# Performance work log

Measured on AMD Instinct MI355X. Metric: run time of the kernel, lower is better.

Reference implementation:

```python
import jax, jax.numpy as jnp
import numpy as np
from jax import lax

B, P, N = 32, 4096, 1024          # batch, phoneme_num, note_num
VOCAB, D, POS = 100, 256, 10      # hp.vocab_size, hp.encoder_dim, pos-emb dim
H = D                             # LSTM hidden size


def conv1d(x, w, b):
    # x: [B, Cin, L], w: [Cout, Cin, 3], padding=1 (same as torch padding=(k-1)//2)
    y = lax.conv_general_dilated(x, w, (1,), [(1, 1)], dimension_numbers=('NCH', 'OIH', 'NCH'))
    return y + b[None, :, None]


def lstm_dir(x, Wih, Whh, bih, bhh, reverse):
    # x: [B, T, I] -> [B, T, H], PyTorch gate order i,f,g,o
    Bn = x.shape[0]
    h0 = jnp.zeros((Bn, H), x.dtype)
    c0 = jnp.zeros((Bn, H), x.dtype)

    def step(carry, xt):
        h, c = carry
        z = xt @ Wih.T + h @ Whh.T + bih + bhh
        i, f, g, o = jnp.split(z, 4, axis=-1)
        c = jax.nn.sigmoid(f) * c + jax.nn.sigmoid(i) * jnp.tanh(g)
        h = jax.nn.sigmoid(o) * jnp.tanh(c)
        return (h, c), h

    _, hs = lax.scan(step, (h0, c0), x.transpose(1, 0, 2), reverse=reverse)
    return hs.transpose(1, 0, 2)


def bilstm(x, wih, whh, bih, bhh):
    f = lstm_dir(x, wih[0], whh[0], bih[0], bhh[0], False)
    b = lstm_dir(x, wih[1], whh[1], bih[1], bhh[1], True)
    return jnp.concatenate([f, b], axis=-1)


def _forward(score_note_dur, phoneme_seq, phoneme_order, emb, pos_emb,
             mix_w1, mix_b1, mix_w2, mix_b2,
             wih0, whh0, bih0, bhh0, wih1, whh1, bih1, bhh1,
             cnn_w1, cnn_b1, cnn_w2, cnn_b2):
    pe = emb[phoneme_seq]            # [B,P,D]
    po = pos_emb[phoneme_order]      # [B,P,10]
    x = jnp.concatenate([pe, po], axis=-1).transpose(0, 2, 1)  # [B,D+10,P]
    x = jax.nn.relu(conv1d(x, mix_w1, mix_b1))
    x = conv1d(x, mix_w2, mix_b2).transpose(0, 2, 1)            # [B,P,D]

    # Vectorized version of the nested note-boundary loop:
    # runs of tokens > 1 map, in order, to notes 0,1,2,...; the last position is
    # never included (torch loop stops at phoneme_end < len-1 and slices [start:end)).
    Lp = phoneme_seq.shape[1]
    valid = phoneme_seq > 1
    valid = valid.at[:, Lp - 1].set(False)
    prev = jnp.pad(valid[:, :-1], ((0, 0), (1, 0)))
    starts = valid & ~prev
    seg = jnp.cumsum(starts.astype(jnp.int32), axis=1) - 1
    seg = jnp.where(valid, seg, N)  # separators / overflow -> dump segment N

    def agg_one(xb, sb):
        s = jax.ops.segment_sum(xb, sb, num_segments=N + 1)
        c = jax.ops.segment_sum(jnp.ones((Lp,), xb.dtype), sb, num_segments=N + 1)
        return s[:N] / jnp.maximum(c[:N, None], 1.0)

    agg = jax.vmap(agg_one)(x, seg)  # [B,N,D]; empty notes stay zero

    d = score_note_dur[..., None]
    enc = jnp.concatenate([agg, d, 1.0 / (d + 1.0)], axis=-1)  # [B,N,D+2]
    y = bilstm(enc, wih0, whh0, bih0, bhh0)
    y = bilstm(y, wih1, whh1, bih1, bhh1)                       # [B,N,2H]
    y = y.transpose(0, 2, 1)
    y = jax.nn.relu(conv1d(y, cnn_w1, cnn_b1))
    y = conv1d(y, cnn_w2, cnn_b2)
    return y.transpose(0, 2, 1)  # [B,N,1]


def setup_inputs() -> dict:
    keys = iter(jax.random.split(jax.random.key(0), 24))

    def nrm(shape, scale):
        return jax.random.normal(next(keys), shape, jnp.float32) * scale

    s = 1.0 / float(np.sqrt(H))
    inp = {}
    inp['score_note_dur'] = jax.random.uniform(next(keys), (B, N), jnp.float32) * 4.0
    inp['phoneme_seq'] = jax.random.randint(next(keys), (B, P), 0, 8)
    inp['phoneme_order'] = jax.random.randint(next(keys), (B, P), 0, 20)
    inp['emb'] = nrm((VOCAB, D), 0.1).at[0].set(0.0)       # padding_idx=0
    inp['pos_emb'] = nrm((20, POS), 0.1).at[0].set(0.0)    # padding_idx=0
    inp['mix_w1'] = nrm((D, D + POS, 3), s)
    inp['mix_b1'] = jnp.zeros((D,), jnp.float32)
    inp['mix_w2'] = nrm((D, D, 3), s)
    inp['mix_b2'] = jnp.zeros((D,), jnp.float32)
    inp['wih0'] = nrm((2, 4 * H, D + 2), s)
    inp['whh0'] = nrm((2, 4 * H, H), s)
    inp['bih0'] = jnp.zeros((2, 4 * H), jnp.float32)
    inp['bhh0'] = jnp.zeros((2, 4 * H), jnp.float32)
    inp['wih1'] = nrm((2, 4 * H, 2 * H), s)
    inp['whh1'] = nrm((2, 4 * H, H), s)
    inp['bih1'] = jnp.zeros((2, 4 * H), jnp.float32)
    inp['bhh1'] = jnp.zeros((2, 4 * H), jnp.float32)
    inp['cnn_w1'] = nrm((D, 2 * H, 3), s)
    inp['cnn_b1'] = jnp.zeros((D,), jnp.float32)
    inp['cnn_w2'] = nrm((1, D, 3), s)
    inp['cnn_b2'] = jnp.zeros((1,), jnp.float32)
    return inp


def reference(score_note_dur, phoneme_seq, phoneme_order, emb, pos_emb,
              mix_w1, mix_b1, mix_w2, mix_b2,
              wih0, whh0, bih0, bhh0, wih1, whh1, bih1, bhh1,
              cnn_w1, cnn_b1, cnn_w2, cnn_b2):
    return _forward(score_note_dur, phoneme_seq, phoneme_order, emb, pos_emb,
                    mix_w1, mix_b1, mix_w2, mix_b2,
                    wih0, whh0, bih0, bhh0, wih1, whh1, bih1, bhh1,
                    cnn_w1, cnn_b1, cnn_w2, cnn_b2)
```

## Files before the change

### kernel.cpp

```cpp
#include <hip/hip_runtime.h>
#include <math.h>

#define B_    32
#define P_    4096
#define N_    1024
#define POS_  10
#define PP    (P_ + 2)
#define NP    (N_ + 2)
#define GB    8
#define NCHK  (B_ / GB)
#define TCH   128
#define NTCH  (N_ / TCH)
#define X0S   280
#define ENCS  288

typedef unsigned short u16;
typedef _Float16 h2_t __attribute__((ext_vector_type(2)));
typedef unsigned u32x4 __attribute__((ext_vector_type(4)));
typedef short s16x8 __attribute__((ext_vector_type(8)));
typedef float f32x4 __attribute__((ext_vector_type(4)));

__device__ __forceinline__ float sigmoidf_(float x) { return 1.f / (1.f + __expf(-x)); }
__device__ __forceinline__ float tanhf_(float x) {
  float t = fminf(fmaxf(x, -30.f), 30.f);
  float e = __expf(2.f * t);
  return (e - 1.f) / (e + 1.f);
}
__device__ __forceinline__ float bf2f(u16 u) { return __uint_as_float(((unsigned)u) << 16); }
__device__ __forceinline__ u16 f2bf(float f) {
  unsigned u = __float_as_uint(f);
  unsigned r = u + 0x7FFFu + ((u >> 16) & 1u);
  return (u16)(r >> 16);
}
__device__ __forceinline__ u16 f2h_bits(float x) {
  _Float16 hh = (_Float16)x; u16 u; __builtin_memcpy(&u, &hh, 2); return u;
}
__device__ __forceinline__ unsigned pack2h(float lo, float hi) {
  return (unsigned)f2h_bits(lo) | ((unsigned)f2h_bits(hi) << 16);
}
__device__ __forceinline__ float dot2(unsigned w, unsigned h, float acc) {
  return __builtin_amdgcn_fdot2(__builtin_bit_cast(h2_t, w), __builtin_bit_cast(h2_t, h), acc, false);
}
#define DOT4(acc, wq, hq) \
  acc = dot2((wq).x, (hq).x, acc); acc = dot2((wq).y, (hq).y, acc); \
  acc = dot2((wq).z, (hq).z, acc); acc = dot2((wq).w, (hq).w, acc);

#define REP24(X) X(0)X(1)X(2)X(3)X(4)X(5)X(6)X(7)X(8)X(9)X(10)X(11)X(12)X(13)X(14)X(15)X(16)X(17)X(18)X(19)X(20)X(21)X(22)X(23)
#define REP8(X)  X(0)X(1)X(2)X(3)X(4)X(5)X(6)X(7)

__device__ __forceinline__ void stc(float* p, float v) { *p = v; }
__device__ __forceinline__ void stc(u16* p, float v)   { *p = f2bf(v); }

__global__ void fill_sentinel_kernel(float* out, int n, float v) {
  int i = blockIdx.x * 256 + threadIdx.x;
  if (i < n) out[i] = v;
}

__global__ void zero_bf_guards_kernel(u16* X0b, u16* X1b) {
  int cb = blockIdx.x, t = threadIdx.x;
  for (int c = t; c < X0S; c += 256) {
    X0b[((long)cb * PP + 0) * X0S + c] = 0;
    X0b[((long)cb * PP + PP - 1) * X0S + c] = 0;
  }
  if (t < 256) {
    X1b[((long)cb * PP + 0) * 256 + t] = 0;
    X1b[((long)cb * PP + PP - 1) * 256 + t] = 0;
  }
}
__global__ void zero_y1p_guards_kernel(u16* Y1p) {
  int b = blockIdx.x, t = threadIdx.x;
  for (int c = t; c < 512; c += 256) {
    Y1p[((long)b * NP + 0) * 512 + c] = 0;
    Y1p[((long)b * NP + NP - 1) * 512 + c] = 0;
  }
}
__global__ void zero_c3p_guards_kernel(float* C3p) {
  int b = blockIdx.x, t = threadIdx.x;
  if (t < 256) {
    C3p[((long)b * NP + 0) * 256 + t] = 0.f;
    C3p[((long)b * NP + NP - 1) * 256 + t] = 0.f;
  }
}

__global__ void embed_bf16_kernel(const int* __restrict__ seq, const int* __restrict__ order,
                                  const float* __restrict__ emb, const float* __restrict__ pos_emb,
                                  u16* __restrict__ X0b, int b0) {
  long i = (long)blockIdx.x * 256 + threadIdx.x;
  const long total = (long)GB * P_ * X0S;
  if (i >= total) return;
  int c = (int)(i % X0S);
  long bp = i / X0S;
  int p = (int)(bp % P_);
  int cb = (int)(bp / P_);
  int b = b0 + cb;
  float v = 0.f;
  if (c < 256)      v = emb[(long)seq[(long)b * P_ + p] * 256 + c];
  else if (c < 266) v = pos_emb[(long)order[(long)b * P_ + p] * POS_ + (c - 256)];
  X0b[((long)cb * PP + p + 1) * X0S + c] = f2bf(v);
}

__global__ void repack_conv_bt_kernel(const float* __restrict__ w, u16* __restrict__ hi,
                                      u16* __restrict__ lo, int CinReal, int strideA,
                                      int Kpad, int Cout) {
  long i = (long)blockIdx.x * 256 + threadIdx.x;
  if (i >= (long)Cout * Kpad) return;
  int co = (int)(i / Kpad), k = (int)(i - (long)co * Kpad);
  int r = k / strideA, ci = k - r * strideA;
  float v = (r < 3 && ci < CinReal) ? w[((long)co * CinReal + ci) * 3 + r] : 0.f;
  u16 h = f2bf(v);
  hi[i] = h;
  if (lo) lo[i] = f2bf(v - bf2f(h));
}
__global__ void repack_dense_bt_kernel(const float* __restrict__ w, u16* __restrict__ hi,
                                       u16* __restrict__ lo, int CinReal, int Kpad) {
  long i = (long)blockIdx.x * 256 + threadIdx.x;
  if (i >= 1024L * Kpad) return;
  int j = (int)(i / Kpad), k = (int)(i - (long)j * Kpad);
  int co = (j & 3) * 256 + (j >> 2);
  float v = (k < CinReal) ? w[(long)co * CinReal + k] : 0.f;
  u16 h = f2bf(v);
  hi[i] = h;
  lo[i] = f2bf(v - bf2f(h));
}
__global__ void repack_whh_reg_kernel(const float* __restrict__ whh, uint4* __restrict__ Wv) {
  long i = (long)blockIdx.x * 256 + threadIdx.x;
  if (i >= 49152) return;
  int j = (int)(i & 511);
  int t = (int)(i >> 9);
  int kq = t % 24, rb = (t / 24) & 1, d = t / 48;
  int R = (j & 3) * 256 + (j >> 2) + rb * 128;
  const float* wr = whh + ((long)d * 1024 + R) * 256;
  uint4 o; unsigned* op = (unsigned*)&o;
#pragma unroll
  for (int q = 0; q < 4; q++) {
    int k = kq * 8 + 2 * q;
    op[q] = pack2h(wr[k], wr[k + 1]);
  }
  Wv[i] = o;
}
__global__ void repack_whh_lds_kernel(const float* __restrict__ whh, uint4* __restrict__ Ws) {
  long i = (long)blockIdx.x * 256 + threadIdx.x;
  if (i >= 16384) return;
  int d = (int)(i >> 13);
  int a = (int)(i & 8191);
  int rb = a >> 12;
  int rem = a & 4095;
  int i2 = rem >> 9, j = rem & 511;
  int R = (j & 3) * 256 + (j >> 2) + rb * 128;
  const float* wr = whh + ((long)d * 1024 + R) * 256;
  uint4 o; unsigned* op = (unsigned*)&o;
#pragma unroll
  for (int q = 0; q < 4; q++) {
    int k = 192 + i2 * 8 + 2 * q;
    op[q] = pack2h(wr[k], wr[k + 1]);
  }
  Ws[i] = o;
}
__global__ void bias_sum_perm_kernel(const float* __restrict__ a, const float* __restrict__ b,
                                     float* __restrict__ dst) {
  int i = blockIdx.x * 256 + threadIdx.x;
  if (i >= 2048) return;
  int d = i >> 10, j = i & 1023;
  int R = (j & 3) * 256 + (j >> 2);
  dst[i] = a[d * 1024 + R] + b[d * 1024 + R];
}
__global__ void repack_conv4_w_kernel(const float* __restrict__ w, float* __restrict__ dst) {
  int i = blockIdx.x * 256 + threadIdx.x;
  if (i < 768) { int r = i >> 8, ci = i & 255; dst[i] = w[ci * 3 + r]; }
}

template <typename CT, bool SPLIT>
__device__ __forceinline__ void gemm_tile(
    int wave, int lane, int bx, int by,
    const u16* __restrict__ A, const u16* __restrict__ Bt, const u16* __restrict__ Bt2,
    const float* __restrict__ bias, CT* __restrict__ C,
    int N, int Kpad, int Mb,
    long aBatchStride, int aRowStride,
    long cBatchStride, int cRowStride, int relu) {
  int lrow = lane & 15, lk = (lane >> 4) * 8;
  int row0 = bx * 64 + wave * 16;
  int col0 = by * 64;
  int grow = row0 + lrow;
  int b_ = grow / Mb, m_ = grow - b_ * Mb;
  const u16* arow = A + (long)b_ * aBatchStride + (long)m_ * aRowStride + lk;
  const u16* bp0 = Bt + (long)(col0 + lrow) * Kpad + lk;
  const u16* bq0 = SPLIT ? (Bt2 + (long)(col0 + lrow) * Kpad + lk) : bp0;
  f32x4 acc0 = {0.f, 0.f, 0.f, 0.f};
  f32x4 acc1 = acc0, acc2 = acc0, acc3 = acc0;
  for (int kk = 0; kk < Kpad; kk += 32) {
    s16x8 av = *(const s16x8*)(arow + kk);
    acc0 = __builtin_amdgcn_mfma_f32_16x16x32_bf16(av, *(const s16x8*)(bp0 + kk), acc0, 0, 0, 0);
    acc1 = __builtin_amdgcn_mfma_f32_16x16x32_bf16(av, *(const s16x8*)(bp0 + 16L * Kpad + kk), acc1, 0, 0, 0);
    acc2 = __builtin_amdgcn_mfma_f32_16x16x32_bf16(av, *(const s16x8*)(bp0 + 32L * Kpad + kk), acc2, 0, 0, 0);
    acc3 = __builtin_amdgcn_mfma_f32_16x16x32_bf16(av, *(const s16x8*)(bp0 + 48L * Kpad + kk), acc3, 0, 0, 0);
    if (SPLIT) {
      acc0 = __builtin_amdgcn_mfma_f32_16x16x32_bf16(av, *(const s16x8*)(bq0 + kk), acc0, 0, 0, 0);
      acc1 = __builtin_amdgcn_mfma_f32_16x16x32_bf16(av, *(const s16x8*)(bq0 + 16L * Kpad + kk), acc1, 0, 0, 0);
      acc2 = __builtin_amdgcn_mfma_f32_16x16x32_bf16(av, *(const s16x8*)(bq0 + 32L * Kpad + kk), acc2, 0, 0, 0);
      acc3 = __builtin_amdgcn_mfma_f32_16x16x32_bf16(av, *(const s16x8*)(bq0 + 48L * Kpad + kk), acc3, 0, 0, 0);
    }
  }
  int erow = row0 + (lane >> 4) * 4;
  int b2 = erow / Mb, m2 = erow - b2 * Mb;
  CT* cbase = C + (long)b2 * cBatchStride + (long)m2 * cRowStride + col0 + lrow;
#define EPI(cc, accv) { \
    float bv = bias[col0 + (cc) * 16 + lrow]; \
    float v0 = accv[0] + bv, v1 = accv[1] + bv, v2 = accv[2] + bv, v3 = accv[3] + bv; \
    if (relu) { v0 = fmaxf(v0, 0.f); v1 = fmaxf(v1, 0.f); v2 = fmaxf(v2, 0.f); v3 = fmaxf(v3, 0.f); } \
    stc(cbase + 0L * cRowStride + (cc) * 16, v0); \
    stc(cbase + 1L * cRowStride + (cc) * 16, v1); \
    stc(cbase + 2L * cRowStride + (cc) * 16, v2); \
    stc(cbase + 3L * cRowStride + (cc) * 16, v3); }
  EPI(0, acc0) EPI(1, acc1) EPI(2, acc2) EPI(3, acc3)
#undef EPI
}

template <typename CT, bool SPLIT>
__global__ __launch_bounds__(256) void gemm_mfma_kernel(
    const u16* __restrict__ A, const u16* __restrict__ Bt, const u16* __restrict__ Bt2,
    const float* __restrict__ bias, CT* __restrict__ C,
    int N, int Kpad, int Mb,
    long aBatchStride, int aRowStride,
    long cBatchStride, int cRowStride, int relu) {
  int tid = threadIdx.x;
  gemm_tile<CT, SPLIT>(tid >> 6, tid & 63, blockIdx.x, blockIdx.y,
                       A, Bt, Bt2, bias, C, N, Kpad, Mb,
                       aBatchStride, aRowStride, cBatchStride, cRowStride, relu);
}

__global__ __launch_bounds__(256) void seg_scan_kernel(const int* __restrict__ seq,
                                int* __restrict__ nstart, int* __restrict__ nlen) {
  __shared__ unsigned char v[P_];
  __shared__ int sc[2][256];
  int b = blockIdx.x, tid = threadIdx.x;
  for (int i = tid; i < P_; i += 256) {
    int s = seq[(long)b * P_ + i];
    v[i] = (s > 1 && i != P_ - 1) ? 1 : 0;
  }
  for (int n = tid; n < N_; n += 256) { nstart[b * N_ + n] = 0; nlen[b * N_ + n] = 0; }
  __syncthreads();
  int base = tid << 4;
  int c = 0;
#pragma unroll
  for (int i = 0; i < 16; i++) {
    int p = base + i;
    int val = v[p];
    int prev = p ? v[p - 1] : 0;
    c += val & (prev ^ 1);
  }
  sc[0][tid] = c;
  __syncthreads();
  int cur = 0;
  for (int d = 1; d < 256; d <<= 1) {
    int x = sc[cur][tid];
    if (tid >= d) x += sc[cur][tid - d];
    sc[cur ^ 1][tid] = x;
    cur ^= 1;
    __syncthreads();
  }
  int sg = tid ? sc[cur][tid - 1] : 0;
  for (int i = 0; i < 16; i++) {
    int p = base + i;
    int val = v[p];
    int prev = p ? v[p - 1] : 0;
    if (val && !prev) {
      if (sg < N_) {
        int len = 0, q = p;
        while (q < P_ && v[q]) { len++; q++; }
        nstart[b * N_ + sg] = p;
        nlen[b * N_ + sg] = len;
      }
      sg++;
    }
  }
}

__global__ __launch_bounds__(256) void agg_enc_kernel(
    const u16* __restrict__ X2b, const int* __restrict__ nstart, const int* __restrict__ nlen,
    const float* __restrict__ dur, u16* __restrict__ enc, int b0) {
  int n = blockIdx.x, gb = blockIdx.y;
  int b = b0 + gb;
  int d = threadIdx.x;
  int len = nlen[b * N_ + n], st = nstart[b * N_ + n];
  float acc = 0.f;
  for (int i = 0; i < len; i++) acc += bf2f(X2b[((long)gb * PP + st + 1 + i) * 256 + d]);
  float m = (len > 0) ? acc / (float)len : 0.f;
  long e = ((long)b * N_ + n) * ENCS;
  enc[e + d] = f2bf(m);
  if (d == 0) {
    float dd = dur[b * N_ + n];
    enc[e + 256] = f2bf(dd);
    enc[e + 257] = f2bf(1.f / (dd + 1.f));
  }
  if (d >= 2 && d < 32) enc[e + 256 + d] = 0;
}

#define REC_LDS_BYTES (131072 + 4096 + 1024)
__global__ __attribute__((amdgpu_waves_per_eu(2, 2))) __launch_bounds__(512)
void rec_gemm_kernel(
    const float* __restrict__ Z,
    const u32x4* __restrict__ Wv,
    const u32x4* __restrict__ Ws,
    float* __restrict__ state,
    u16* __restrict__ Y, int yRowsPerB, int yPad, int r,
    const u16* __restrict__ Xg, const u16* __restrict__ Whg, const u16* __restrict__ Wlg,
    const float* __restrict__ bsg, float* __restrict__ Zg, int Kpg, int rq) {
  int tid = threadIdx.x;
  if (blockIdx.x >= 64) {
    int half = tid >> 8, vt = tid & 255;
    int tile = (blockIdx.x - 64) * 2 + half;
    int dir = tile >> 10;
    int t2 = tile & 1023;
    int bx = t2 & 63, by = t2 >> 6;
    int t0g = (dir == 0) ? rq * TCH : (NTCH - 1 - rq) * TCH;
    long WihD = (long)1024 * Kpg;
    long ZD = (long)B_ * TCH * 1024;
    gemm_tile<float, true>((vt >> 6), vt & 63, bx, by,
        Xg + (long)t0g * Kpg, Whg + (long)dir * WihD, Wlg + (long)dir * WihD,
        bsg + dir * 1024, Zg + (long)dir * ZD,
        1024, Kpg, TCH, (long)N_ * Kpg, Kpg, (long)TCH * 1024, 1024, 0);
    return;
  }
  extern __shared__ char smem[];
  u32x4* WL = (u32x4*)smem;
  float* zb = (float*)(smem + 131072);
  u16*   hb = (u16*)(smem + 131072 + 4096);
  const u32x4* hb4 = (const u32x4*)hb;

  int chain = blockIdx.x;
  int d = chain >> 5, b = chain & 31;
  const float* Zb = Z + (long)(d * 32 + b) * (TCH * 1024);

  for (int iq = 0; iq < 16; ++iq) {
    int q = iq * 512 + tid;
    WL[q] = Ws[(long)d * 8192 + q];
  }
  const u32x4* WvD = Wv + (long)d * 2 * 24 * 512;
#define DECLW(i) u32x4 wA##i, wB##i;
  REP24(DECLW)
#undef DECLW
#define LOADW(i) wA##i = WvD[(i) * 512 + tid]; wB##i = WvD[(24 + (i)) * 512 + tid];
  REP24(LOADW)
#undef LOADW
#define PINW(i) asm volatile("" : "+v"(wA##i), "+v"(wB##i));
  REP24(PINW)
#undef PINW

  float h_reg = 0.f, c_reg = 0.f;
  if (tid < 256) {
    if (r > 0) {
      h_reg = state[(chain * 2 + 0) * 256 + tid];
      c_reg = state[(chain * 2 + 1) * 256 + tid];
    }
    hb[tid] = f2h_bits(h_reg);
  }
  __syncthreads();

  int t0 = (d == 0) ? r * TCH : (NTCH - 1 - r) * TCH;
  int tcf = d ? (TCH - 1) : 0;
  float preA = Zb[(long)tcf * 1024 + tid];
  float preB = Zb[(long)tcf * 1024 + 512 + tid];

  for (int tt = 0; tt < TCH; ++tt) {
    float accA = preA, accB = preB;
    if (tt + 1 < TCH) {
      int tc2 = d ? (TCH - 2 - tt) : (tt + 1);
      preA = Zb[(long)tc2 * 1024 + tid];
      preB = Zb[(long)tc2 * 1024 + 512 + tid];
    }
#define MACW(i) { u32x4 hq = hb4[i]; DOT4(accA, wA##i, hq); DOT4(accB, wB##i, hq); }
    REP24(MACW)
#undef MACW
#define MACL(i) { u32x4 hq = hb4[24 + (i)]; \
                  u32x4 qa = WL[(i) * 512 + tid]; \
                  u32x4 qb = WL[4096 + (i) * 512 + tid]; \
                  DOT4(accA, qa, hq); DOT4(accB, qb, hq); }
    REP8(MACL)
#undef MACL
    zb[tid] = accA;
    zb[tid + 512] = accB;
    __syncthreads();
    int tcur = d ? (TCH - 1 - tt) : tt;
    if (tid < 256) {
      float4 z4 = *(const float4*)&zb[tid * 4];
      float ig = sigmoidf_(z4.x), fg = sigmoidf_(z4.y);
      float gg = tanhf_(z4.z), og = sigmoidf_(z4.w);
      c_reg = fg * c_reg + ig * gg;
      float h = og * tanhf_(c_reg);
      h_reg = h;
      hb[tid] = f2h_bits(h);
      Y[((long)b * yRowsPerB + t0 + tcur + yPad) * 512 + d * 256 + tid] = f2bf(h);
    }
    __syncthreads();
  }
  if (r != NTCH - 1 && tid < 256) {
    state[(chain * 2 + 0) * 256 + tid] = h_reg;
    state[(chain * 2 + 1) * 256 + tid] = c_reg;
  }
}

__global__ __launch_bounds__(256) void conv4_kernel(
    const float* __restrict__ C3p, const float* __restrict__ w,
    const float* __restrict__ b2, float* __restrict__ out) {
  int row = blockIdx.x * 4 + (threadIdx.x >> 6);
  int lane = threadIdx.x & 63;
  int b = row >> 10, t = row & (N_ - 1);
  const float* a = C3p + ((long)b * NP + t) * 256;
  float acc = 0.f;
  for (int k = lane; k < 768; k += 64) acc += a[k] * w[k];
  for (int off = 32; off; off >>= 1) acc += __shfl_down(acc, off, 64);
  if (lane == 0) out[row] = acc + b2[0];
}

extern "C" void kernel_launch(void* const* d_in, const int* in_sizes, int n_in,
                              void* d_out, int out_size, void* d_ws, size_t ws_size,
                              hipStream_t stream) {
  const float* dur     = (const float*)d_in[0];
  const int*   seq     = (const int*)d_in[1];
  const int*   order   = (const int*)d_in[2];
  const float* emb     = (const float*)d_in[3];
  const float* pos_emb = (const float*)d_in[4];
  const float* mix_w1  = (const float*)d_in[5];
  const float* mix_b1  = (const float*)d_in[6];
  const float* mix_w2  = (const float*)d_in[7];
  const float* mix_b2  = (const float*)d_in[8];
  const float* wih0    = (const float*)d_in[9];
  const float* whh0    = (const float*)d_in[10];
  const float* bih0    = (const float*)d_in[11];
  const float* bhh0    = (const float*)d_in[12];
  const float* wih1    = (const float*)d_in[13];
  const float* whh1    = (const float*)d_in[14];
  const float* bih1    = (const float*)d_in[15];
  const float* bhh1    = (const float*)d_in[16];
  const float* cnn_w1  = (const float*)d_in[17];
  const float* cnn_b1  = (const float*)d_in[18];
  const float* cnn_w2  = (const float*)d_in[19];
  const float* cnn_b2  = (const float*)d_in[20];
  float* out = (float*)d_out;
  float* ws = (float*)d_ws;

  (void)hipFuncSetAttribute((const void*)rec_gemm_kernel,
                            hipFuncAttributeMaxDynamicSharedMemorySize, REC_LDS_BYTES);

  const long X0B_F = (long)GB * PP * X0S / 2;
  const long X1B_F = (long)GB * PP * 256 / 2;
  const long X2B_F = X1B_F;
  const long ZE2   = 2L * B_ * TCH * 1024;
  const long C3P_E = (long)B_ * NP * 256;
  long region = X0B_F + X1B_F + X2B_F;
  if (2 * ZE2 > region) region = 2 * ZE2;
  if (C3P_E > region) region = C3P_E;

  long off = 0;
  auto alloc = [&](long n) { long ret = off; off += (n + 15) & ~15L; return ret; };
  long o_region = alloc(region);
  long o_enc    = alloc((long)B_ * N_ * ENCS / 2);
  long o_Y0     = alloc((long)B_ * N_ * 512 / 2);
  long o_Y1p    = alloc((long)B_ * NP * 512 / 2);
  long o_W1h    = alloc(256L * 832 / 2);
  long o_W2h    = alloc(256L * 768 / 2);
  long o_Wc1h   = alloc(256L * 1536 / 2);
  long o_Wc1l   = alloc(256L * 1536 / 2);
  long o_Wc2r   = alloc(768);
  long o_Wih0h  = alloc(2L * 1024 * ENCS / 2);
  long o_Wih0l  = alloc(2L * 1024 * ENCS / 2);
  long o_Wih1h  = alloc(2L * 1024 * 512 / 2);
  long o_Wih1l  = alloc(2L * 1024 * 512 / 2);
  long o_Wv0    = alloc(49152L * 4);
  long o_Ws0    = alloc(16384L * 4);
  long o_Wv1    = alloc(49152L * 4);
  long o_Ws1    = alloc(16384L * 4);
  long o_bs0    = alloc(2048);
  long o_bs1    = alloc(2048);
  long o_state  = alloc(64L * 2 * 256);
  long o_nst    = alloc((long)B_ * N_);
  long o_nln    = alloc((long)B_ * N_);

  if ((size_t)(off * 4) > ws_size) {
    float v = -(1000.0f + (float)(ws_size >> 20));
    fill_sentinel_kernel<<<(out_size + 255) / 256, 256, 0, stream>>>(out, out_size, v);
    return;
  }

  u16*   X0b  = (u16*)(ws + o_region);
  u16*   X1b  = (u16*)(ws + o_region + X0B_F);
  u16*   X2b  = (u16*)(ws + o_region + X0B_F + X1B_F);
  float* Zbuf[2] = { ws + o_region, ws + o_region + ZE2 };
  float* C3p  = ws + o_region;
  u16*   enc  = (u16*)(ws + o_enc);
  u16*   Y0   = (u16*)(ws + o_Y0);
  u16*   Y1p  = (u16*)(ws + o_Y1p);
  u16*   W1h  = (u16*)(ws + o_W1h);
  u16*   W2h  = (u16*)(ws + o_W2h);
  u16*   Wc1h = (u16*)(ws + o_Wc1h);
  u16*   Wc1l = (u16*)(ws + o_Wc1l);
  float* Wc2r = ws + o_Wc2r;
  u16*   Wih0h = (u16*)(ws + o_Wih0h);
  u16*   Wih0l = (u16*)(ws + o_Wih0l);
  u16*   Wih1h = (u16*)(ws + o_Wih1h);
  u16*   Wih1l = (u16*)(ws + o_Wih1l);
  uint4* Wv0  = (uint4*)(ws + o_Wv0);
  uint4* Ws0  = (uint4*)(ws + o_Ws0);
  uint4* Wv1  = (uint4*)(ws + o_Wv1);
  uint4* Ws1  = (uint4*)(ws + o_Ws1);
  float* bs0  = ws + o_bs0;
  float* bs1  = ws + o_bs1;
  float* state = ws + o_state;
  int* nstart = (int*)(ws + o_nst);
  int* nlen   = (int*)(ws + o_nln);

  zero_bf_guards_kernel<<<GB, 256, 0, stream>>>(X0b, X1b);
  zero_y1p_guards_kernel<<<B_, 256, 0, stream>>>(Y1p);
  repack_conv_bt_kernel<<<(int)((256L * 832 + 255) / 256), 256, 0, stream>>>(
      mix_w1, W1h, nullptr, 266, X0S, 832, 256);
  repack_conv_bt_kernel<<<(int)((256L * 768 + 255) / 256), 256, 0, stream>>>(
      mix_w2, W2h, nullptr, 256, 256, 768, 256);
  repack_conv_bt_kernel<<<(int)((256L * 1536 + 255) / 256), 256, 0, stream>>>(
      cnn_w1, Wc1h, Wc1l, 512, 512, 1536, 256);
  repack_conv4_w_kernel<<<3, 256, 0, stream>>>(cnn_w2, Wc2r);
  for (int d = 0; d < 2; d++) {
    repack_dense_bt_kernel<<<(int)((1024L * ENCS + 255) / 256), 256, 0, stream>>>(
        wih0 + (long)d * 1024 * 258, Wih0h + (long)d * 1024 * ENCS,
        Wih0l + (long)d * 1024 * ENCS, 258, ENCS);
    repack_dense_bt_kernel<<<(int)((1024L * 512 + 255) / 256), 256, 0, stream>>>(
        wih1 + (long)d * 1024 * 512, Wih1h + (long)d * 1024 * 512,
        Wih1l + (long)d * 1024 * 512, 512, 512);
  }
  repack_whh_reg_kernel<<<192, 256, 0, stream>>>(whh0, Wv0);
  repack_whh_lds_kernel<<<64, 256, 0, stream>>>(whh0, Ws0);
  repack_whh_reg_kernel<<<192, 256, 0, stream>>>(whh1, Wv1);
  repack_whh_lds_kernel<<<64, 256, 0, stream>>>(whh1, Ws1);
  bias_sum_perm_kernel<<<8, 256, 0, stream>>>(bih0, bhh0, bs0);
  bias_sum_perm_kernel<<<8, 256, 0, stream>>>(bih1, bhh1, bs1);
  seg_scan_kernel<<<B_, 256, 0, stream>>>(seq, nstart, nlen);

  for (int ch = 0; ch < NCHK; ch++) {
    int b0 = ch * GB;
    long total = (long)GB * P_ * X0S;
    embed_bf16_kernel<<<(int)((total + 255) / 256), 256, 0, stream>>>(seq, order, emb, pos_emb, X0b, b0);
    gemm_mfma_kernel<u16, false><<<dim3(GB * P_ / 64, 4), 256, 0, stream>>>(
        X0b, W1h, nullptr, mix_b1, X1b + 256,
        256, 832, P_, (long)PP * X0S, X0S, (long)PP * 256, 256, 1);
    gemm_mfma_kernel<u16, false><<<dim3(GB * P_ / 64, 4), 256, 0, stream>>>(
        X1b, W2h, nullptr, mix_b2, X2b + 256,
        256, 768, P_, (long)PP * 256, 256, (long)PP * 256, 256, 0);
    agg_enc_kernel<<<dim3(N_, GB), 256, 0, stream>>>(X2b, nstart, nlen, dur, enc, b0);
  }

  const long ZD = (long)B_ * TCH * 1024;
  for (int layer = 0; layer < 2; layer++) {
    const u16*  Xl   = (layer == 0) ? enc : Y0;
    int         Kp   = (layer == 0) ? ENCS : 512;
    const u16*  Wh   = (layer == 0) ? Wih0h : Wih1h;
    const u16*  Wl   = (layer == 0) ? Wih0l : Wih1l;
    long        WihD = (long)1024 * Kp;
    const float* bsl = (layer == 0) ? bs0 : bs1;
    const u32x4* Wv  = (const u32x4*)((layer == 0) ? Wv0 : Wv1);
    const u32x4* Wsp = (const u32x4*)((layer == 0) ? Ws0 : Ws1);
    u16*        Yl   = (layer == 0) ? Y0 : Y1p;
    int         yRows = (layer == 0) ? N_ : NP;
    int         yPad  = (layer == 0) ? 0 : 1;
    for (int d = 0; d < 2; d++) {
      int t0 = (d == 0) ? 0 : (NTCH - 1) * TCH;
      gemm_mfma_kernel<float, true><<<dim3(B_ * TCH / 64, 16), 256, 0, stream>>>(
          Xl + (long)t0 * Kp, Wh + (long)d * WihD, Wl + (long)d * WihD,
          bsl + d * 1024, Zbuf[0] + d * ZD,
          1024, Kp, TCH, (long)N_ * Kp, Kp, (long)TCH * 1024, 1024, 0);
    }
    for (int r = 0; r < NTCH; r++) {
      int gemmWGs = (r < NTCH - 1) ? 1024 : 0;
      rec_gemm_kernel<<<64 + gemmWGs, 512, REC_LDS_BYTES, stream>>>(
          Zbuf[r & 1], Wv, Wsp, state, Yl, yRows, yPad, r,
          Xl, Wh, Wl, bsl, Zbuf[(r + 1) & 1], Kp, r + 1);
    }
  }

  zero_c3p_guards_kernel<<<B_, 256, 0, stream>>>(C3p);
  gemm_mfma_kernel<float, true><<<dim3(B_ * N_ / 64, 4), 256, 0, stream>>>(
      Y1p, Wc1h, Wc1l, cnn_b1, C3p + 256,
      256, 1536, N_, (long)NP * 512, 512, (long)NP * 256, 256, 1);
  conv4_kernel<<<B_ * N_ / 4, 256, 0, stream>>>(C3p, Wc2r, cnn_b2, out);
}
```

Baseline: 5.402 ms.

## Stage GEMM A/B tiles through LDS instead of direct global fragment loads

The MFMA GEMM tile previously had every wave load its own A and B fragments straight from global memory, so each B row was fetched once per wave. It now loads 64x32 tiles of A, B-high and B-low cooperatively into padded LDS (80-byte rows) and reads the MFMA fragments from there. This is meant to cut redundant global traffic. The cost is two __syncthreads per K step with no double buffering. The GEMM blocks fused into the recurrent kernel reuse the dynamic shared memory for their tiles.

```diff
diff --git a/kernel.cpp b/kernel.cpp
--- a/kernel.cpp
+++ b/kernel.cpp
@@ -13,6 +13,9 @@
 #define NTCH  (N_ / TCH)
 #define X0S   280
 #define ENCS  288
+#define LROW  80
+#define LTILE (64 * LROW)
+#define GEMM_LDS (3 * LTILE)
 
 typedef unsigned short u16;
 typedef _Float16 h2_t __attribute__((ext_vector_type(2)));
@@ -170,37 +173,55 @@
 }
 
 template <typename CT, bool SPLIT>
-__device__ __forceinline__ void gemm_tile(
-    int wave, int lane, int bx, int by,
+__device__ __forceinline__ void gemm_tile_lds(
+    char* smbase, int tid, int bx, int by,
     const u16* __restrict__ A, const u16* __restrict__ Bt, const u16* __restrict__ Bt2,
     const float* __restrict__ bias, CT* __restrict__ C,
     int N, int Kpad, int Mb,
     long aBatchStride, int aRowStride,
     long cBatchStride, int cRowStride, int relu) {
-  int lrow = lane & 15, lk = (lane >> 4) * 8;
-  int row0 = bx * 64 + wave * 16;
-  int col0 = by * 64;
-  int grow = row0 + lrow;
-  int b_ = grow / Mb, m_ = grow - b_ * Mb;
-  const u16* arow = A + (long)b_ * aBatchStride + (long)m_ * aRowStride + lk;
-  const u16* bp0 = Bt + (long)(col0 + lrow) * Kpad + lk;
-  const u16* bq0 = SPLIT ? (Bt2 + (long)(col0 + lrow) * Kpad + lk) : bp0;
+  char* As = smbase;
+  char* Bh = smbase + LTILE;
+  char* Bl = smbase + 2 * LTILE;
+  int wave = tid >> 6, lane = tid & 63;
+  int lrow = lane & 15, lkg = lane >> 4;
+  int row0 = bx * 64, col0 = by * 64;
+  int srow = tid >> 2, skoff = (tid & 3) * 8;
+  int sgrow = row0 + srow;
+  int sb = sgrow / Mb, smr = sgrow - sb * Mb;
+  const u16* gA  = A + (long)sb * aBatchStride + (long)smr * aRowStride + skoff;
+  const u16* gBh = Bt + (long)(col0 + srow) * Kpad + skoff;
+  const u16* gBl = SPLIT ? (Bt2 + (long)(col0 + srow) * Kpad + skoff) : gBh;
+  int wb = srow * LROW + (tid & 3) * 16;
+  int frow = wave * 16 + lrow;
+  int ab  = frow * LROW + lkg * 16;
+  int bb0 = lrow * LROW + lkg * 16;
+
   f32x4 acc0 = {0.f, 0.f, 0.f, 0.f};
   f32x4 acc1 = acc0, acc2 = acc0, acc3 = acc0;
   for (int kk = 0; kk < Kpad; kk += 32) {
-    s16x8 av = *(const s16x8*)(arow + kk);
-    acc0 = __builtin_amdgcn_mfma_f32_16x16x32_bf16(av, *(const s16x8*)(bp0 + kk), acc0, 0, 0, 0);
-    acc1 = __builtin_amdgcn_mfma_f32_16x16x32_bf16(av, *(const s16x8*)(bp0 + 16L * Kpad + kk), acc1, 0, 0, 0);
-    acc2 = __builtin_amdgcn_mfma_f32_16x16x32_bf16(av, *(const s16x8*)(bp0 + 32L * Kpad + kk), acc2, 0, 0, 0);
-    acc3 = __builtin_amdgcn_mfma_f32_16x16x32_bf16(av, *(const s16x8*)(bp0 + 48L * Kpad + kk), acc3, 0, 0, 0);
+    s16x8 ra  = *(const s16x8*)(gA + kk);
+    s16x8 rbh = *(const s16x8*)(gBh + kk);
+    s16x8 rbl;
+    if (SPLIT) rbl = *(const s16x8*)(gBl + kk);
+    __syncthreads();
+    *(s16x8*)(As + wb) = ra;
+    *(s16x8*)(Bh + wb) = rbh;
+    if (SPLIT) *(s16x8*)(Bl + wb) = rbl;
+    __syncthreads();
+    s16x8 av = *(const s16x8*)(As + ab);
+    acc0 = __builtin_amdgcn_mfma_f32_16x16x32_bf16(av, *(const s16x8*)(Bh + bb0 + 0 * (16 * LROW)), acc0, 0, 0, 0);
+    acc1 = __builtin_amdgcn_mfma_f32_16x16x32_bf16(av, *(const s16x8*)(Bh + bb0 + 1 * (16 * LROW)), acc1, 0, 0, 0);
+    acc2 = __builtin_amdgcn_mfma_f32_16x16x32_bf16(av, *(const s16x8*)(Bh + bb0 + 2 * (16 * LROW)), acc2, 0, 0, 0);
+    acc3 = __builtin_amdgcn_mfma_f32_16x16x32_bf16(av, *(const s16x8*)(Bh + bb0 + 3 * (16 * LROW)), acc3, 0, 0, 0);
     if (SPLIT) {
-      acc0 = __builtin_amdgcn_mfma_f32_16x16x32_bf16(av, *(const s16x8*)(bq0 + kk), acc0, 0, 0, 0);
-      acc1 = __builtin_amdgcn_mfma_f32_16x16x32_bf16(av, *(const s16x8*)(bq0 + 16L * Kpad + kk), acc1, 0, 0, 0);
-      acc2 = __builtin_amdgcn_mfma_f32_16x16x32_bf16(av, *(const s16x8*)(bq0 + 32L * Kpad + kk), acc2, 0, 0, 0);
-      acc3 = __builtin_amdgcn_mfma_f32_16x16x32_bf16(av, *(const s16x8*)(bq0 + 48L * Kpad + kk), acc3, 0, 0, 0);
+      acc0 = __builtin_amdgcn_mfma_f32_16x16x32_bf16(av, *(const s16x8*)(Bl + bb0 + 0 * (16 * LROW)), acc0, 0, 0, 0);
+      acc1 = __builtin_amdgcn_mfma_f32_16x16x32_bf16(av, *(const s16x8*)(Bl + bb0 + 1 * (16 * LROW)), acc1, 0, 0, 0);
+      acc2 = __builtin_amdgcn_mfma_f32_16x16x32_bf16(av, *(const s16x8*)(Bl + bb0 + 2 * (16 * LROW)), acc2, 0, 0, 0);
+      acc3 = __builtin_amdgcn_mfma_f32_16x16x32_bf16(av, *(const s16x8*)(Bl + bb0 + 3 * (16 * LROW)), acc3, 0, 0, 0);
     }
   }
-  int erow = row0 + (lane >> 4) * 4;
+  int erow = row0 + wave * 16 + lkg * 4;
   int b2 = erow / Mb, m2 = erow - b2 * Mb;
   CT* cbase = C + (long)b2 * cBatchStride + (long)m2 * cRowStride + col0 + lrow;
 #define EPI(cc, accv) { \
@@ -222,10 +243,10 @@
     int N, int Kpad, int Mb,
     long aBatchStride, int aRowStride,
     long cBatchStride, int cRowStride, int relu) {
-  int tid = threadIdx.x;
-  gemm_tile<CT, SPLIT>(tid >> 6, tid & 63, blockIdx.x, blockIdx.y,
-                       A, Bt, Bt2, bias, C, N, Kpad, Mb,
-                       aBatchStride, aRowStride, cBatchStride, cRowStride, relu);
+  __shared__ char smtile[GEMM_LDS];
+  gemm_tile_lds<CT, SPLIT>(smtile, threadIdx.x, blockIdx.x, blockIdx.y,
+                           A, Bt, Bt2, bias, C, N, Kpad, Mb,
+                           aBatchStride, aRowStride, cBatchStride, cRowStride, relu);
 }
 
 __global__ __launch_bounds__(256) void seg_scan_kernel(const int* __restrict__ seq,
@@ -305,6 +326,7 @@
     u16* __restrict__ Y, int yRowsPerB, int yPad, int r,
     const u16* __restrict__ Xg, const u16* __restrict__ Whg, const u16* __restrict__ Wlg,
     const float* __restrict__ bsg, float* __restrict__ Zg, int Kpg, int rq) {
+  extern __shared__ char smem[];
   int tid = threadIdx.x;
   if (blockIdx.x >= 64) {
     int half = tid >> 8, vt = tid & 255;
@@ -315,13 +337,12 @@
     int t0g = (dir == 0) ? rq * TCH : (NTCH - 1 - rq) * TCH;
     long WihD = (long)1024 * Kpg;
     long ZD = (long)B_ * TCH * 1024;
-    gemm_tile<float, true>((vt >> 6), vt & 63, bx, by,
+    gemm_tile_lds<float, true>(smem + half * GEMM_LDS, vt, bx, by,
         Xg + (long)t0g * Kpg, Whg + (long)dir * WihD, Wlg + (long)dir * WihD,
         bsg + dir * 1024, Zg + (long)dir * ZD,
         1024, Kpg, TCH, (long)N_ * Kpg, Kpg, (long)TCH * 1024, 1024, 0);
     return;
   }
-  extern __shared__ char smem[];
   u32x4* WL = (u32x4*)smem;
   float* zb = (float*)(smem + 131072);
   u16*   hb = (u16*)(smem + 131072 + 4096);
```

Result: faster. 4.421 ms (median of 3 runs) (-18.2%).
